# Kernel tuning notes

Hardware: AMD Instinct MI355X
Metric: run time of the kernel (lower is better)

## Reference

```python
import jax, jax.numpy as jnp
import numpy as np

N = 100000      # nodes
E = 1600000     # edges (avg degree 16)
F = 128         # nfeats
H = 4           # nheads
D = 16          # nhid // nheads
ALPHA = 0.2     # LeakyReLU negative slope


def setup_inputs() -> dict:
    key = jax.random.key(0)
    k0, k1, k2, k3, k4 = jax.random.split(key, 5)
    h = jax.random.normal(k0, (N, F), dtype=jnp.float32)
    src = jax.random.randint(k1, (E,), 0, N)
    dst = jax.random.randint(k2, (E,), 0, N)
    # per-head Linear W (xavier_uniform gain=1.414 approx) and attention vector a
    limW = 1.414 * np.sqrt(6.0 / (F + D))
    W = jax.random.uniform(k3, (H, F, D), jnp.float32, -limW, limW)
    Wb = jnp.zeros((H, D), jnp.float32)
    lima = 1.414 * np.sqrt(6.0 / (2 * D + 1))
    a = jax.random.uniform(k4, (H, 2 * D), jnp.float32, -lima, lima)
    ab = jnp.zeros((H,), jnp.float32)
    return {"h": h, "W": W, "Wb": Wb, "a": a, "ab": ab, "src": src, "dst": dst}


def reference(h, W, Wb, a, ab, src, dst):
    # Per-head linear projection (dropout is identity in eval mode)
    Wh = jnp.einsum('nf,hfd->nhd', h, W) + Wb          # [N,H,D]
    Whs = Wh[src]                                       # [E,H,D] gather src
    Whd = Wh[dst]                                       # [E,H,D] gather dst
    # e = leakyrelu(a . [Wh_src || Wh_dst])
    e = (jnp.einsum('ehd,hd->eh', Whs, a[:, :D]) +
         jnp.einsum('ehd,hd->eh', Whd, a[:, D:]) + ab)  # [E,H]
    e = jnp.where(e > 0, e, ALPHA * e)
    # segment softmax over incoming edges per dst node
    m = jax.ops.segment_max(e, dst, num_segments=N)     # [N,H]
    m = jnp.where(jnp.isfinite(m), m, 0.0)
    p = jnp.exp(e - m[dst])                             # [E,H]
    denom = jax.ops.segment_sum(p, dst, num_segments=N) # [N,H]
    num = jax.ops.segment_sum(p[:, :, None] * Whs, dst, num_segments=N)  # [N,H,D]
    h_prime = num / jnp.maximum(denom, 1e-9)[:, :, None]
    # concat heads -> [N, H*D]; rows of nodes with no in-edges are zero
    return h_prime.reshape(N, H * D)
```

## Files before the change

kernel.cpp:

```cpp
#include <hip/hip_runtime.h>
#include <hip/hip_bf16.h>
#include <math.h>

#define N_NODES 100000
#define N_EDGES 1600000
#define NF 128
#define NH 4
#define ND 16
#define GAT_ALPHA 0.2f

#define BSHIFT 8
#define NBK 391
#define CAPB 5120
#define EPB 8192

typedef __attribute__((ext_vector_type(8))) __bf16 bf16x8;
typedef __attribute__((ext_vector_type(4))) float f32x4;

#define PADK 136
#define NTILES ((N_NODES + 63) / 64)

__device__ __forceinline__ uint pack2_bf16(float x, float y)
{
    __hip_bfloat162 t = __float22bfloat162_rn(make_float2(x, y));
    return *reinterpret_cast<uint*>(&t);
}

__global__ __launch_bounds__(256, 4) void k_project_mfma(
    const float* __restrict__ h, const float* __restrict__ W,
    const float* __restrict__ Wb, const float* __restrict__ a,
    const float* __restrict__ ab, __hip_bfloat16* __restrict__ Whb,
    float* __restrict__ es, float* __restrict__ ed)
{
    __shared__ __align__(16) __hip_bfloat16 Bt[80 * PADK];
    __shared__ __align__(16) __hip_bfloat16 At[64 * PADK];

    const int tid = threadIdx.x;
    const int wv = tid >> 6;
    const int l = tid & 63;
    const int m = l & 15;
    const int quad = l >> 4;

    for (int idx = tid; idx < 64 * 128; idx += 256) {
        int d = idx & 15, hh = (idx >> 4) & 3, f = idx >> 6;
        Bt[(hh * 16 + d) * PADK + f] =
            __float2bfloat16(W[hh * (NF * ND) + f * ND + d]);
    }
    for (int idx = tid; idx < 128 * 4; idx += 256) {
        int f = idx >> 2, hh = idx & 3;
        float s1 = 0.f, s2 = 0.f;
        #pragma unroll
        for (int d = 0; d < 16; d++) {
            float wv_ = W[hh * (NF * ND) + f * ND + d];
            s1 = fmaf(wv_, a[hh * 32 + d], s1);
            s2 = fmaf(wv_, a[hh * 32 + 16 + d], s2);
        }
        Bt[(64 + hh) * PADK + f] = __float2bfloat16(s1);
        Bt[(72 + hh) * PADK + f] = __float2bfloat16(s2);
    }
    for (int idx = tid; idx < 8 * 128; idx += 256) {
        int f = idx & 127, c = idx >> 7;
        int n = (c < 4) ? (68 + c) : (72 + c);
        Bt[n * PADK + f] = __float2bfloat16(0.f);
    }

    float wb4[4];
    #pragma unroll
    for (int t = 0; t < 4; t++) wb4[t] = Wb[t * 16 + m];
    float eb = 0.f;
    if (m < 4) {
        #pragma unroll
        for (int d = 0; d < 16; d++) eb = fmaf(Wb[m * 16 + d], a[m * 32 + d], eb);
    } else if (m >= 8 && m < 12) {
        int hh = m - 8;
        #pragma unroll
        for (int d = 0; d < 16; d++)
            eb = fmaf(Wb[hh * 16 + d], a[hh * 32 + 16 + d], eb);
        eb += ab[hh];
    }

    for (int tile = blockIdx.x; tile < NTILES; tile += gridDim.x) {
        const int tb = tile * 64;
        __syncthreads();
        #pragma unroll
        for (int i = 0; i < 8; i++) {
            int fidx = tid + i * 256;
            int row = fidx >> 5, f4 = fidx & 31;
            int node = tb + row;
            float4 v = make_float4(0.f, 0.f, 0.f, 0.f);
            if (node < N_NODES) v = ((const float4*)h)[node * 32 + f4];
            uint2 p;
            p.x = pack2_bf16(v.x, v.y);
            p.y = pack2_bf16(v.z, v.w);
            *(uint2*)&At[row * PADK + f4 * 4] = p;
        }
        __syncthreads();

        f32x4 acc[5];
        #pragma unroll
        for (int t = 0; t < 5; t++) acc[t] = (f32x4){0.f, 0.f, 0.f, 0.f};

        const int arow = (wv * 16 + m) * PADK;
        #pragma unroll
        for (int kk = 0; kk < 4; kk++) {
            bf16x8 af = *(const bf16x8*)&At[arow + kk * 32 + quad * 8];
            #pragma unroll
            for (int t = 0; t < 5; t++) {
                bf16x8 bf = *(const bf16x8*)&Bt[(t * 16 + m) * PADK + kk * 32 + quad * 8];
                acc[t] = __builtin_amdgcn_mfma_f32_16x16x32_bf16(af, bf, acc[t], 0, 0, 0);
            }
        }

        const int nodeb = tb + wv * 16 + quad * 4;
        #pragma unroll
        for (int r = 0; r < 4; r++) {
            int node = nodeb + r;
            if (node < N_NODES) {
                #pragma unroll
                for (int t = 0; t < 4; t++)
                    Whb[node * 64 + t * 16 + m] = __float2bfloat16(acc[t][r] + wb4[t]);
                float ev = acc[4][r] + eb;
                if (m < 4) es[node * 4 + m] = ev;
                else if (m >= 8 && m < 12) ed[node * 4 + (m - 8)] = ev;
            }
        }
    }
}

__device__ __forceinline__ int block_scan_incl(int v, int* wsum)
{
    int lane = threadIdx.x & 63, wid = threadIdx.x >> 6;
    int x = v;
    #pragma unroll
    for (int o = 1; o < 64; o <<= 1) {
        int y = __shfl_up(x, o);
        if (lane >= o) x += y;
    }
    if (lane == 63) wsum[wid] = x;
    __syncthreads();
    int add = 0;
    for (int k = 0; k < wid; k++) add += wsum[k];
    return x + add;
}

__global__ __launch_bounds__(256) void k_bplace(
    const int* __restrict__ src, const int* __restrict__ dst,
    int* __restrict__ gcur, uint* __restrict__ sb)
{
    __shared__ int hist[NBK];
    __shared__ int cur[NBK];
    const int t = threadIdx.x;
    const int base = blockIdx.x * EPB;
    const int lim = min(EPB, N_EDGES - base);

    for (int i = t; i < NBK; i += 256) hist[i] = 0;
    __syncthreads();
    for (int i = t; i < lim; i += 256)
        atomicAdd(&hist[dst[base + i] >> BSHIFT], 1);
    __syncthreads();
    for (int i = t; i < NBK; i += 256) {
        int v = hist[i];
        cur[i] = v ? atomicAdd(&gcur[i], v) : 0;
    }
    __syncthreads();
    for (int i = t; i < lim; i += 256) {
        int d = dst[base + i];
        int bk = d >> BSHIFT;
        int pos = atomicAdd(&cur[bk], 1);
        if (pos < CAPB)
            sb[bk * CAPB + pos] = (uint)(src[base + i] | ((d & 255) << 17));
    }
}

__global__ __launch_bounds__(256) void k_csr(
    const uint* __restrict__ sb, const int* __restrict__ gcur,
    int* __restrict__ cnt, int* __restrict__ off, int* __restrict__ ssrc)
{
    __shared__ int ncnt[256];
    __shared__ int ncur[256];
    __shared__ int wsum[8];
    const int b = blockIdx.x;
    const int ebase = b * CAPB;
    const int ecnt = min(gcur[b], CAPB);
    const int t = threadIdx.x;

    ncnt[t] = 0;
    __syncthreads();
    for (int i = t; i < ecnt; i += 256)
        atomicAdd(&ncnt[sb[ebase + i] >> 17], 1);
    __syncthreads();
    int s = ncnt[t];
    int incl = block_scan_incl(s, wsum);
    int excl = incl - s;
    ncur[t] = excl;
    int node = b * 256 + t;
    if (node < N_NODES) {
        cnt[node] = s;
        off[node] = ebase + excl;
    }
    __syncthreads();
    for (int i = t; i < ecnt; i += 256) {
        uint v = sb[ebase + i];
        int pos = atomicAdd(&ncur[v >> 17], 1);
        ssrc[ebase + pos] = (int)(v & 0x1FFFFu);
    }
}

__global__ __launch_bounds__(256) void k_gather(
    const __hip_bfloat16* __restrict__ Whb, const float* __restrict__ es,
    const float* __restrict__ ed, const int* __restrict__ off,
    const int* __restrict__ cnt, const int* __restrict__ ssrc,
    float* __restrict__ out)
{
    __shared__ int   s_lds[4][64];
    __shared__ float p_lds[4][256];
    const int wid = threadIdx.x >> 6;
    const int l = threadIdx.x & 63;
    const int r = l & 15;
    const int q = l >> 4;
    const int hh = r >> 2;

    const int n = blockIdx.x * 4 + wid;
    const int start = off[n];
    const int deg = cnt[n];

    const float4 edv = ((const float4*)ed)[n];
    const float4* es4 = (const float4*)es;
    const uint2* Wu2 = (const uint2*)Whb;

    int* su = &s_lds[wid][0];
    float* pu = &p_lds[wid][0];
    const int* su_q = su + q;
    const float* pu_q = pu + q * 4 + hh;

    float acc0 = 0.f, acc1 = 0.f, acc2 = 0.f, acc3 = 0.f, den = 0.f;

    for (int b = 0; b < deg; b += 64) {
        int rem = deg - b;
        int nchunk = rem < 64 ? rem : 64;

        int sl = 0;
        float4 p4 = make_float4(0.f, 0.f, 0.f, 0.f);
        if (l < nchunk) {
            sl = ssrc[start + b + l];
            float4 esv = es4[sl];
            float x;
            x = esv.x + edv.x; p4.x = __expf(fmaxf(x, GAT_ALPHA * x));
            x = esv.y + edv.y; p4.y = __expf(fmaxf(x, GAT_ALPHA * x));
            x = esv.z + edv.z; p4.z = __expf(fmaxf(x, GAT_ALPHA * x));
            x = esv.w + edv.w; p4.w = __expf(fmaxf(x, GAT_ALPHA * x));
        }
        su[l] = sl;
        ((float4*)pu)[l] = p4;

        #pragma unroll 4
        for (int jj = 0; jj < nchunk; jj += 4) {
            int s = su_q[jj];
            float p = pu_q[jj * 4];
            uint2 v = Wu2[s * 16 + r];
            acc0 = fmaf(p, __uint_as_float(v.x << 16), acc0);
            acc1 = fmaf(p, __uint_as_float(v.x & 0xffff0000u), acc1);
            acc2 = fmaf(p, __uint_as_float(v.y << 16), acc2);
            acc3 = fmaf(p, __uint_as_float(v.y & 0xffff0000u), acc3);
            den += p;
        }
    }

    acc0 += __shfl_xor(acc0, 16); acc1 += __shfl_xor(acc1, 16);
    acc2 += __shfl_xor(acc2, 16); acc3 += __shfl_xor(acc3, 16);
    den  += __shfl_xor(den, 16);
    acc0 += __shfl_xor(acc0, 32); acc1 += __shfl_xor(acc1, 32);
    acc2 += __shfl_xor(acc2, 32); acc3 += __shfl_xor(acc3, 32);
    den  += __shfl_xor(den, 32);

    if (q == 0) {
        float rr = 1.0f / fmaxf(den, 1e-9f);
        ((float4*)out)[n * 16 + r] =
            make_float4(acc0 * rr, acc1 * rr, acc2 * rr, acc3 * rr);
    }
}

extern "C" void kernel_launch(void* const* d_in, const int* in_sizes, int n_in,
                              void* d_out, int out_size, void* d_ws, size_t ws_size,
                              hipStream_t stream)
{
    const float* h  = (const float*)d_in[0];
    const float* W  = (const float*)d_in[1];
    const float* Wb = (const float*)d_in[2];
    const float* a  = (const float*)d_in[3];
    const float* ab = (const float*)d_in[4];
    const int* src  = (const int*)d_in[5];
    const int* dst  = (const int*)d_in[6];
    float* out = (float*)d_out;

    char* w = (char*)d_ws;
    __hip_bfloat16* Whb = (__hip_bfloat16*)w; w += (size_t)N_NODES * 64 * 2;
    float* es      = (float*)w;  w += (size_t)N_NODES * 4 * 4;
    float* ed      = (float*)w;  w += (size_t)N_NODES * 4 * 4;
    int* cnt       = (int*)w;    w += (size_t)N_NODES * 4;
    int* off       = (int*)w;    w += (size_t)N_NODES * 4;
    uint* sb       = (uint*)w;   w += (size_t)NBK * CAPB * 4;
    int* ssrc      = (int*)w;    w += (size_t)NBK * CAPB * 4;
    int* gcur      = (int*)w;    w += 512 * 4;

    hipMemsetAsync(gcur, 0, NBK * sizeof(int), stream);
    k_bplace<<<(N_EDGES + EPB - 1) / EPB, 256, 0, stream>>>(src, dst, gcur, sb);
    k_csr<<<NBK, 256, 0, stream>>>(sb, gcur, cnt, off, ssrc);
    k_project_mfma<<<782, 256, 0, stream>>>(h, W, Wb, a, ab, Whb, es, ed);
    k_gather<<<N_NODES / 4, 256, 0, stream>>>(Whb, es, ed, off, cnt, ssrc, out);
}
```

Measured before the change: 217.5 us.

## Fuse edge bucket placement and MFMA projection into one heterogeneous kernel

Merges the edge-bucketing kernel and the projection kernel into a single launch. The first 196 blocks do bucket placement and the remaining blocks do the projection, so the two independent stages run concurrently and one launch is removed. The projection now loads h rows straight from global memory into MFMA A-fragments instead of staging them through LDS, which also drops a shared buffer and a barrier. The risks are that direct per-lane float4 loads are less coalesced, and that the min-blocks launch bound is gone, which may change occupancy.

```diff
diff --git a/kernel.cpp b/kernel.cpp
--- a/kernel.cpp
+++ b/kernel.cpp
@@ -13,29 +13,54 @@
 #define NBK 391
 #define CAPB 5120
 #define EPB 8192
+#define EBLK 196
+#define PBLK 782
+#define NTILES ((N_NODES + 63) / 64)
 
 typedef __attribute__((ext_vector_type(8))) __bf16 bf16x8;
 typedef __attribute__((ext_vector_type(4))) float f32x4;
 
 #define PADK 136
-#define NTILES ((N_NODES + 63) / 64)
-
-__device__ __forceinline__ uint pack2_bf16(float x, float y)
-{
-    __hip_bfloat162 t = __float22bfloat162_rn(make_float2(x, y));
-    return *reinterpret_cast<uint*>(&t);
-}
-
-__global__ __launch_bounds__(256, 4) void k_project_mfma(
+
+__global__ __launch_bounds__(256) void k_fused(
     const float* __restrict__ h, const float* __restrict__ W,
     const float* __restrict__ Wb, const float* __restrict__ a,
-    const float* __restrict__ ab, __hip_bfloat16* __restrict__ Whb,
+    const float* __restrict__ ab, const int* __restrict__ src,
+    const int* __restrict__ dst, int* __restrict__ gcur,
+    uint* __restrict__ sb, __hip_bfloat16* __restrict__ Whb,
     float* __restrict__ es, float* __restrict__ ed)
 {
     __shared__ __align__(16) __hip_bfloat16 Bt[80 * PADK];
-    __shared__ __align__(16) __hip_bfloat16 At[64 * PADK];
+    __shared__ int hist[NBK];
+    __shared__ int cur[NBK];
 
     const int tid = threadIdx.x;
+
+    if (blockIdx.x < EBLK) {
+        const int base = blockIdx.x * EPB;
+        const int lim = min(EPB, N_EDGES - base);
+
+        for (int i = tid; i < NBK; i += 256) hist[i] = 0;
+        __syncthreads();
+        for (int i = tid; i < lim; i += 256)
+            atomicAdd(&hist[dst[base + i] >> BSHIFT], 1);
+        __syncthreads();
+        for (int i = tid; i < NBK; i += 256) {
+            int v = hist[i];
+            cur[i] = v ? atomicAdd(&gcur[i], v) : 0;
+        }
+        __syncthreads();
+        for (int i = tid; i < lim; i += 256) {
+            int d = dst[base + i];
+            int bk = d >> BSHIFT;
+            int pos = atomicAdd(&cur[bk], 1);
+            if (pos < CAPB)
+                sb[bk * CAPB + pos] = (uint)(src[base + i] | ((d & 255) << 17));
+        }
+        return;
+    }
+
+    const int pb = blockIdx.x - EBLK;
     const int wv = tid >> 6;
     const int l = tid & 63;
     const int m = l & 15;
@@ -78,32 +103,31 @@
             eb = fmaf(Wb[hh * 16 + d], a[hh * 32 + 16 + d], eb);
         eb += ab[hh];
     }
-
-    for (int tile = blockIdx.x; tile < NTILES; tile += gridDim.x) {
-        const int tb = tile * 64;
-        __syncthreads();
-        #pragma unroll
-        for (int i = 0; i < 8; i++) {
-            int fidx = tid + i * 256;
-            int row = fidx >> 5, f4 = fidx & 31;
-            int node = tb + row;
-            float4 v = make_float4(0.f, 0.f, 0.f, 0.f);
-            if (node < N_NODES) v = ((const float4*)h)[node * 32 + f4];
-            uint2 p;
-            p.x = pack2_bf16(v.x, v.y);
-            p.y = pack2_bf16(v.z, v.w);
-            *(uint2*)&At[row * PADK + f4 * 4] = p;
-        }
-        __syncthreads();
+    __syncthreads();
+
+    for (int tile = pb; tile < NTILES; tile += PBLK) {
+        const int node = tile * 64 + wv * 16 + m;
+        const bool ok = node < N_NODES;
+        const float4* hrow = (const float4*)(h + (size_t)(ok ? node : 0) * NF);
 
         f32x4 acc[5];
         #pragma unroll
         for (int t = 0; t < 5; t++) acc[t] = (f32x4){0.f, 0.f, 0.f, 0.f};
 
-        const int arow = (wv * 16 + m) * PADK;
         #pragma unroll
         for (int kk = 0; kk < 4; kk++) {
-            bf16x8 af = *(const bf16x8*)&At[arow + kk * 32 + quad * 8];
+            bf16x8 af;
+            if (ok) {
+                float4 v0 = hrow[kk * 8 + quad * 2];
+                float4 v1 = hrow[kk * 8 + quad * 2 + 1];
+                af[0] = (__bf16)v0.x; af[1] = (__bf16)v0.y;
+                af[2] = (__bf16)v0.z; af[3] = (__bf16)v0.w;
+                af[4] = (__bf16)v1.x; af[5] = (__bf16)v1.y;
+                af[6] = (__bf16)v1.z; af[7] = (__bf16)v1.w;
+            } else {
+                #pragma unroll
+                for (int j = 0; j < 8; j++) af[j] = (__bf16)0.f;
+            }
             #pragma unroll
             for (int t = 0; t < 5; t++) {
                 bf16x8 bf = *(const bf16x8*)&Bt[(t * 16 + m) * PADK + kk * 32 + quad * 8];
@@ -111,17 +135,17 @@
             }
         }
 
-        const int nodeb = tb + wv * 16 + quad * 4;
+        const int nodeb = tile * 64 + wv * 16 + quad * 4;
         #pragma unroll
         for (int r = 0; r < 4; r++) {
-            int node = nodeb + r;
-            if (node < N_NODES) {
+            int n = nodeb + r;
+            if (n < N_NODES) {
                 #pragma unroll
                 for (int t = 0; t < 4; t++)
-                    Whb[node * 64 + t * 16 + m] = __float2bfloat16(acc[t][r] + wb4[t]);
+                    Whb[n * 64 + t * 16 + m] = __float2bfloat16(acc[t][r] + wb4[t]);
                 float ev = acc[4][r] + eb;
-                if (m < 4) es[node * 4 + m] = ev;
-                else if (m >= 8 && m < 12) ed[node * 4 + (m - 8)] = ev;
+                if (m < 4) es[n * 4 + m] = ev;
+                else if (m >= 8 && m < 12) ed[n * 4 + (m - 8)] = ev;
             }
         }
     }
@@ -141,35 +165,6 @@
     int add = 0;
     for (int k = 0; k < wid; k++) add += wsum[k];
     return x + add;
-}
-
-__global__ __launch_bounds__(256) void k_bplace(
-    const int* __restrict__ src, const int* __restrict__ dst,
-    int* __restrict__ gcur, uint* __restrict__ sb)
-{
-    __shared__ int hist[NBK];
-    __shared__ int cur[NBK];
-    const int t = threadIdx.x;
-    const int base = blockIdx.x * EPB;
-    const int lim = min(EPB, N_EDGES - base);
-
-    for (int i = t; i < NBK; i += 256) hist[i] = 0;
-    __syncthreads();
-    for (int i = t; i < lim; i += 256)
-        atomicAdd(&hist[dst[base + i] >> BSHIFT], 1);
-    __syncthreads();
-    for (int i = t; i < NBK; i += 256) {
-        int v = hist[i];
-        cur[i] = v ? atomicAdd(&gcur[i], v) : 0;
-    }
-    __syncthreads();
-    for (int i = t; i < lim; i += 256) {
-        int d = dst[base + i];
-        int bk = d >> BSHIFT;
-        int pos = atomicAdd(&cur[bk], 1);
-        if (pos < CAPB)
-            sb[bk * CAPB + pos] = (uint)(src[base + i] | ((d & 255) << 17));
-    }
 }
 
 __global__ __launch_bounds__(256) void k_csr(
@@ -304,8 +299,8 @@
     int* gcur      = (int*)w;    w += 512 * 4;
 
     hipMemsetAsync(gcur, 0, NBK * sizeof(int), stream);
-    k_bplace<<<(N_EDGES + EPB - 1) / EPB, 256, 0, stream>>>(src, dst, gcur, sb);
+    k_fused<<<EBLK + PBLK, 256, 0, stream>>>(h, W, Wb, a, ab, src, dst,
+                                             gcur, sb, Whb, es, ed);
     k_csr<<<NBK, 256, 0, stream>>>(sb, gcur, cnt, off, ssrc);
-    k_project_mfma<<<782, 256, 0, stream>>>(h, W, Wb, a, ab, Whb, es, ed);
     k_gather<<<N_NODES / 4, 256, 0, stream>>>(Whb, es, ed, off, cnt, ssrc, out);
 }
```

Result: faster. 209.2 us (-3.8%).
